# Kernel tuning notes

Hardware: AMD Instinct MI355X
Metric: run time of the kernel (lower is better)

Reference implementation:

```python
import jax, jax.numpy as jnp
import numpy as np

NUM_HEADS = 16

def _rope_tables(T, head_dim):
    # angular_freq: (1/1024)**linspace(0,1,head_dim//4), padded with head_dim//4 zeros
    af = (1.0 / 1024.0) ** jnp.linspace(0.0, 1.0, head_dim // 4, dtype=jnp.float32)
    af = jnp.concatenate([af, jnp.zeros(head_dim // 4, dtype=jnp.float32)])  # [head_dim//2]
    t = jnp.arange(T, dtype=jnp.float32)
    theta = t[:, None] * af[None, :]  # [T, head_dim//2]
    return jnp.cos(theta), jnp.sin(theta)

def _apply_rope(x_bthd, cos, sin):
    # x_bthd: [B,T,H,D]; cos/sin: [T,D//2]
    x1, x2 = jnp.split(x_bthd.astype(jnp.float32), 2, axis=-1)
    c = cos[None, :, None, :]
    s = sin[None, :, None, :]
    y1 = x1 * c + x2 * s
    y2 = -x1 * s + x2 * c
    return jnp.concatenate([y1, y2], axis=-1).astype(x_bthd.dtype)

def setup_inputs() -> dict:
    key = jax.random.key(0)
    k1, k2, k3 = jax.random.split(key, 3)
    B, T, C = 4, 2048, 1024
    std = 0.5 * C ** (-0.5)
    bound = (3.0 ** 0.5) * std
    x = jax.random.normal(k1, (B, T, C), dtype=jnp.float32)
    qkv_w = jax.random.uniform(k2, (3, C, C), dtype=jnp.float32, minval=-bound, maxval=bound)
    c_proj_w = 0.02 * jax.random.normal(k3, (C, C), dtype=jnp.float32)
    c_proj_b = jnp.zeros((C,), dtype=jnp.float32)
    return {"x": x, "qkv_w": qkv_w, "c_proj_w": c_proj_w, "c_proj_b": c_proj_b}

def reference(x, qkv_w, c_proj_w, c_proj_b):
    B, T, C = x.shape
    H = NUM_HEADS
    D = C // H
    # QKV projection: F.linear(x, qkv_w.flatten(end_dim=1)) -> x @ W.T
    qkv = jnp.einsum('btc,nc->btn', x, qkv_w.reshape(3 * C, C))  # [B,T,3C]
    qkv = qkv.reshape(B, T, 3 * H, D)
    q, k, v = jnp.split(qkv, 3, axis=-2)  # each [B,T,H,D]
    cos, sin = _rope_tables(T, D)
    q = _apply_rope(q, cos, sin)
    k = _apply_rope(k, cos, sin)
    # causal SDPA, scale 1/sqrt(D)
    scale = 1.0 / jnp.sqrt(jnp.float32(D))
    scores = jnp.einsum('bqhd,bkhd->bhqk', q, k) * scale  # [B,H,T,T]
    mask = jnp.tril(jnp.ones((T, T), dtype=bool))
    scores = jnp.where(mask[None, None], scores, jnp.finfo(scores.dtype).min)
    attn = jax.nn.softmax(scores, axis=-1)
    y = jnp.einsum('bhqk,bkhd->bqhd', attn, v).reshape(B, T, C)
    return y @ c_proj_w.T + c_proj_b
```

## Files before the change

kernel.cpp:

```cpp
#include <hip/hip_runtime.h>

typedef unsigned short ushort_t;
typedef __bf16 bf16x8 __attribute__((ext_vector_type(8)));
typedef unsigned short ushort8_t __attribute__((ext_vector_type(8)));
typedef unsigned short ushort4_t __attribute__((ext_vector_type(4)));
typedef float floatx4 __attribute__((ext_vector_type(4)));
typedef unsigned int uint4_t __attribute__((ext_vector_type(4)));
typedef unsigned int uint2_t __attribute__((ext_vector_type(2)));

__device__ __forceinline__ ushort_t f2bf(float f) {
    unsigned int u = __float_as_uint(f);
    u += 0x7FFFu + ((u >> 16) & 1u);
    return (ushort_t)(u >> 16);
}
__device__ __forceinline__ float bf2f(ushort_t b) {
    return __uint_as_float(((unsigned int)b) << 16);
}
__device__ __forceinline__ bf16x8 ld_frag(const ushort_t* p) {
    ushort8_t u = *(const ushort8_t*)p;
    return __builtin_bit_cast(bf16x8, u);
}
__device__ __forceinline__ unsigned pack_trunc(float lo, float hi) {
    return __builtin_amdgcn_perm(__float_as_uint(hi), __float_as_uint(lo), 0x07060302u);
}
__device__ __forceinline__ floatx4 mfma16(bf16x8 a, bf16x8 b, floatx4 c) {
    return __builtin_amdgcn_mfma_f32_16x16x32_bf16(a, b, c, 0, 0, 0);
}
__device__ __forceinline__ void async16(const ushort_t* g, ushort_t* l) {
    __builtin_amdgcn_global_load_lds((const __attribute__((address_space(1))) void*)g,
                                     (__attribute__((address_space(3))) void*)l, 16, 0, 0);
}

__global__ __launch_bounds__(256) void cvt_dual(const float* __restrict__ s1,
                                                ushort_t* __restrict__ d1, int n1,
                                                const float* __restrict__ s2,
                                                ushort_t* __restrict__ d2, int n2) {
    int idx = blockIdx.x * 256 + threadIdx.x;
    const float* src;
    ushort_t* dst;
    if (idx < n1) {
        src = s1; dst = d1;
    } else {
        idx -= n1;
        if (idx >= n2) return;
        src = s2; dst = d2;
    }
    const float4* s = (const float4*)src + (size_t)idx * 2;
    float4 a = s[0], b = s[1];
    ushort8_t v;
    v[0] = f2bf(a.x); v[1] = f2bf(a.y); v[2] = f2bf(a.z); v[3] = f2bf(a.w);
    v[4] = f2bf(b.x); v[5] = f2bf(b.y); v[6] = f2bf(b.z); v[7] = f2bf(b.w);
    *(ushort8_t*)(dst + (size_t)idx * 8) = v;
}

template <int MODE>
__global__ __launch_bounds__(256) void gemm_a(const ushort_t* __restrict__ A,
                                              const ushort_t* __restrict__ B,
                                              const float* __restrict__ bias,
                                              void* __restrict__ Cout,
                                              ushort_t* __restrict__ vt,
                                              int M, int N) {
    constexpr int K = 1024;
    __shared__ __attribute__((aligned(16))) ushort_t As[128 * 32];
    __shared__ __attribute__((aligned(16))) ushort_t Bs[128 * 32];
    const int tid = threadIdx.x;
    const int lane = tid & 63, wave = tid >> 6;
    const int quad = lane >> 4, l16 = lane & 15;
    const int wm = wave & 1, wn = wave >> 1;
    const int m0 = blockIdx.y * 128, n0 = blockIdx.x * 128;

    const ushort_t* ga = A + (size_t)(m0 + wave * 32 + (lane >> 2)) * K + (lane & 3) * 8;
    const ushort_t* gb = B + (size_t)(n0 + wave * 32 + (lane >> 2)) * K + (lane & 3) * 8;
    const ushort_t* ga2 = ga + 16 * K;
    const ushort_t* gb2 = gb + 16 * K;
    ushort_t* la = As + wave * 1024;
    ushort_t* lb = Bs + wave * 1024;

    floatx4 acc[4][4] = {};

#pragma unroll
    for (int k0 = 0; k0 < K; k0 += 32) {
        __syncthreads();
        async16(ga + k0, la);
        async16(ga2 + k0, la + 512);
        async16(gb + k0, lb);
        async16(gb2 + k0, lb + 512);
        __syncthreads();

        bf16x8 af[4], bfr[4];
#pragma unroll
        for (int mt = 0; mt < 4; ++mt)
            af[mt] = ld_frag(&As[(wm * 64 + mt * 16 + l16) * 32 + quad * 8]);
#pragma unroll
        for (int nt = 0; nt < 4; ++nt)
            bfr[nt] = ld_frag(&Bs[(wn * 64 + nt * 16 + l16) * 32 + quad * 8]);
#pragma unroll
        for (int mt = 0; mt < 4; ++mt)
#pragma unroll
            for (int nt = 0; nt < 4; ++nt)
                acc[mt][nt] = mfma16(af[mt], bfr[nt], acc[mt][nt]);
    }

    if constexpr (MODE == 2) {
        if (n0 + wn * 64 < 2048) {
            float afreq = exp2f((float)l16 * (-10.0f / 15.0f));
#pragma unroll
            for (int mt = 0; mt < 4; ++mt) {
                int rowb = m0 + wm * 64 + mt * 16 + quad * 4;
#pragma unroll
                for (int r = 0; r < 4; ++r) {
                    int t = (rowb + r) & 2047;
                    float th = (float)t * afreq;
                    float sn, cs;
                    __sincosf(th, &sn, &cs);
                    float q1 = acc[mt][0][r], q2 = acc[mt][2][r];
                    acc[mt][0][r] = q1 * cs + q2 * sn;
                    acc[mt][2][r] = -q1 * sn + q2 * cs;
                }
            }
        }
    }

#pragma unroll
    for (int mt = 0; mt < 4; ++mt) {
        int row = m0 + wm * 64 + mt * 16 + quad * 4;
#pragma unroll
        for (int nt = 0; nt < 4; ++nt) {
            int nglob = n0 + wn * 64 + nt * 16 + l16;
            if constexpr (MODE == 0) {
                float bv = bias ? bias[nglob] : 0.0f;
#pragma unroll
                for (int r = 0; r < 4; ++r)
                    ((float*)Cout)[(size_t)(row + r) * N + nglob] = acc[mt][nt][r] + bv;
            } else {
                if (nglob < 2048) {
#pragma unroll
                    for (int r = 0; r < 4; ++r)
                        ((ushort_t*)Cout)[(size_t)(row + r) * 2048 + nglob] =
                            f2bf(acc[mt][nt][r]);
                } else {
                    int d = nglob & 63, hh = (nglob >> 6) & 15;
                    int bb = row >> 11, t = row & 2047;
                    ushort4_t pk;
                    pk.x = f2bf(acc[mt][nt][0]);
                    pk.y = f2bf(acc[mt][nt][1]);
                    pk.z = f2bf(acc[mt][nt][2]);
                    pk.w = f2bf(acc[mt][nt][3]);
                    *(ushort4_t*)&vt[(((size_t)bb * 16 + hh) * 64 + d) * 2048 + t] = pk;
                }
            }
        }
    }
}

#define ATT_SCALE 0.18033688011112042f

template <bool DIAG>
__device__ __forceinline__ void attn_step(
    const ushort_t* __restrict__ Ks, const ushort_t* __restrict__ Vt,
    ushort_t* __restrict__ Pw, const bf16x8 (&qf)[2][2],
    floatx4 (&o)[2][4], floatx4 (&lac)[2], float (&m_)[2],
    int quad, int l16, int sw8, int mhi, int qrel) {
    ushort8_t ou;
#pragma unroll
    for (int j = 0; j < 8; ++j) ou[j] = 0x3F80;
    const bf16x8 vONE = __builtin_bit_cast(bf16x8, ou);

    floatx4 s[8][2];
    __builtin_amdgcn_s_setprio(1);
#pragma unroll
    for (int mt = 0; mt < 8; ++mt) {
        if (DIAG && mt > mhi) continue;
        const ushort_t* kr = &Ks[(mt * 16 + l16) * 64];
        bf16x8 k0 = ld_frag(kr + ((quad * 8) ^ sw8));
        bf16x8 k1 = ld_frag(kr + ((32 + quad * 8) ^ sw8));
#pragma unroll
        for (int nt = 0; nt < 2; ++nt) {
            floatx4 z = {};
            z = mfma16(k0, qf[nt][0], z);
            s[mt][nt] = mfma16(k1, qf[nt][1], z);
        }
    }
    __builtin_amdgcn_s_setprio(0);

    if (DIAG) {
#pragma unroll
        for (int mt = 0; mt < 8; ++mt) {
            if (mt > mhi) continue;
#pragma unroll
            for (int nt = 0; nt < 2; ++nt)
#pragma unroll
                for (int r = 0; r < 4; ++r)
                    if (mt * 16 + quad * 4 + r > qrel + nt * 16 + l16)
                        s[mt][nt][r] = -3e38f;
        }
    }

    float mx[2];
#pragma unroll
    for (int nt = 0; nt < 2; ++nt) {
        float m0 = -3e38f;
#pragma unroll
        for (int mt = 0; mt < 8; ++mt) {
            if (DIAG && mt > mhi) continue;
            m0 = fmaxf(m0, fmaxf(fmaxf(s[mt][nt][0], s[mt][nt][1]),
                                 fmaxf(s[mt][nt][2], s[mt][nt][3])));
        }
        m0 = fmaxf(m0, __shfl_xor(m0, 16));
        m0 = fmaxf(m0, __shfl_xor(m0, 32));
        mx[nt] = m0;
    }
    bool resc = !__all((mx[0] - m_[0] <= 8.0f) && (mx[1] - m_[1] <= 8.0f));
    if (resc) {
        float alpha_l[2];
#pragma unroll
        for (int nt = 0; nt < 2; ++nt) {
            float mnew = fmaxf(m_[nt], mx[nt]);
            alpha_l[nt] = __builtin_amdgcn_exp2f(m_[nt] - mnew);
            m_[nt] = mnew;
        }
#pragma unroll
        for (int mtq = 0; mtq < 2; ++mtq)
#pragma unroll
            for (int r = 0; r < 4; ++r) {
                float ao = __shfl(alpha_l[mtq], quad * 4 + r);
                lac[mtq][r] *= ao;
#pragma unroll
                for (int ntd = 0; ntd < 4; ++ntd) o[mtq][ntd][r] *= ao;
            }
    }
#pragma unroll
    for (int nt = 0; nt < 2; ++nt)
#pragma unroll
        for (int mt = 0; mt < 8; ++mt) {
            if (DIAG && mt > mhi) continue;
#pragma unroll
            for (int r = 0; r < 4; ++r)
                s[mt][nt][r] = __builtin_amdgcn_exp2f(s[mt][nt][r] - m_[nt]);
        }

#pragma unroll
    for (int half = 0; half < 2; ++half) {
        if (DIAG && 4 * half > mhi) continue;
#pragma unroll
        for (int mt = 4 * half; mt < 4 * half + 4; ++mt) {
            if (DIAG && mt > mhi) continue;
#pragma unroll
            for (int nt = 0; nt < 2; ++nt) {
                uint2_t pk;
                pk.x = pack_trunc(s[mt][nt][0], s[mt][nt][1]);
                pk.y = pack_trunc(s[mt][nt][2], s[mt][nt][3]);
                *(uint2_t*)&Pw[(nt * 16 + l16) * 72 + (mt - 4 * half) * 16 + quad * 4] =
                    pk;
            }
        }

        __builtin_amdgcn_s_setprio(1);
#pragma unroll
        for (int kc2 = 0; kc2 < 2; ++kc2) {
            const int kc = 2 * half + kc2;
            if (DIAG && kc > (mhi >> 1)) continue;
            bf16x8 ap0 = ld_frag(&Pw[l16 * 72 + kc2 * 32 + quad * 8]);
            bf16x8 ap1 = ld_frag(&Pw[(16 + l16) * 72 + kc2 * 32 + quad * 8]);
            lac[0] = mfma16(ap0, vONE, lac[0]);
            lac[1] = mfma16(ap1, vONE, lac[1]);
#pragma unroll
            for (int ntd = 0; ntd < 4; ++ntd) {
                bf16x8 bv = ld_frag(&Vt[(ntd * 16 + l16) * 136 + kc * 32 + quad * 8]);
                o[0][ntd] = mfma16(ap0, bv, o[0][ntd]);
                o[1][ntd] = mfma16(ap1, bv, o[1][ntd]);
            }
        }
        __builtin_amdgcn_s_setprio(0);
    }
}

__global__ __launch_bounds__(256, 2) void attn_kernel(const ushort_t* __restrict__ qk,
                                                      const ushort_t* __restrict__ vt,
                                                      ushort_t* __restrict__ y) {
    __shared__ __attribute__((aligned(16))) ushort_t Ks[128 * 64];
    __shared__ __attribute__((aligned(16))) ushort_t Vt[64 * 136];
    __shared__ __attribute__((aligned(16))) ushort_t Pw_all[4 * 2304];

    const int tid = threadIdx.x, lane = tid & 63, w = tid >> 6;
    const int quad = lane >> 4, l16 = lane & 15;
    const int lrow = lane >> 3, lchunk = lane & 7;
    const int sw8 = 8 * (l16 >> 1);
    ushort_t* Pw = Pw_all + w * 2304;

    const int idx = (int)blockIdx.x;
    const int rank = idx >> 6, bh = idx & 63;
    constexpr int jj_tab[16] = {15, 13, 11, 9, 0, 2, 4, 6, 14, 12, 10, 8, 1, 3, 5, 7};
    const int jj = jj_tab[rank];
    const int b = bh >> 4, h = bh & 15;

    const ushort_t* base_k = qk + (size_t)(b * 2048) * 2048 + 1024 + h * 64;
    const ushort_t* base_v = vt + (size_t)bh * 64 * 2048;
    const int vd = w * 4 + (lane >> 4);
    const int vc8 = lane & 15;

    ushort8_t kreg[4], vreg[4];
    auto load_kv = [&](int kt) {
        const ushort_t* gk = base_k + (size_t)(kt * 128) * 2048 + lchunk * 8;
#pragma unroll
        for (int i = 0; i < 4; ++i)
            kreg[i] = *(const ushort8_t*)(gk + (size_t)(w * 32 + i * 8 + lrow) * 2048);
        const ushort_t* gv = base_v + kt * 128;
#pragma unroll
        for (int i = 0; i < 4; ++i)
            vreg[i] = *(const ushort8_t*)(gv + (size_t)(i * 16 + vd) * 2048 + vc8 * 8);
    };
    auto store_kv = [&]() {
#pragma unroll
        for (int i = 0; i < 4; ++i) {
            int row = w * 32 + i * 8 + lrow;
            *(ushort8_t*)&Ks[row * 64 + 8 * (lchunk ^ ((row >> 1) & 7))] = kreg[i];
        }
#pragma unroll
        for (int i = 0; i < 4; ++i)
            *(ushort8_t*)&Vt[(i * 16 + vd) * 136 + vc8 * 8] = vreg[i];
    };

    const int q0 = jj * 128 + w * 32;

    bf16x8 qf[2][2];
    {
        const ushort_t* qb = qk + (size_t)(b * 2048 + q0) * 2048 + h * 64 + quad * 8;
#pragma unroll
        for (int nt = 0; nt < 2; ++nt)
#pragma unroll
            for (int kd = 0; kd < 2; ++kd) {
                ushort8_t raw =
                    *(const ushort8_t*)(qb + (size_t)(nt * 16 + l16) * 2048 + kd * 32);
                uint4_t dw;
#pragma unroll
                for (int jx = 0; jx < 4; ++jx) {
                    float f0 = bf2f(raw[2 * jx]) * ATT_SCALE;
                    float f1 = bf2f(raw[2 * jx + 1]) * ATT_SCALE;
                    dw[jx] = pack_trunc(f0, f1);
                }
                qf[nt][kd] = __builtin_bit_cast(bf16x8, dw);
            }
    }

    floatx4 o[2][4] = {};
    floatx4 lac[2] = {};
    float m_[2] = {-3e38f, -3e38f};

    load_kv(0);
#pragma unroll 1
    for (int kt = 0; kt <= jj; ++kt) {
        __syncthreads();
        store_kv();
        __syncthreads();
        if (kt < jj) load_kv(kt + 1);

        if (kt < jj)
            attn_step<false>(Ks, Vt, Pw, qf, o, lac, m_, quad, l16, sw8, 7, 0);
        else
            attn_step<true>(Ks, Vt, Pw, qf, o, lac, m_, quad, l16, sw8, 2 * w + 1,
                            w * 32);
    }

    ushort_t* yb = y + (size_t)(b * 2048 + q0) * 1024 + h * 64;
#pragma unroll
    for (int mtq = 0; mtq < 2; ++mtq)
#pragma unroll
        for (int r = 0; r < 4; ++r) {
            float inv = 1.0f / lac[mtq][r];
            int row = mtq * 16 + quad * 4 + r;
#pragma unroll
            for (int ntd = 0; ntd < 4; ++ntd)
                yb[(size_t)row * 1024 + ntd * 16 + l16] = f2bf(o[mtq][ntd][r] * inv);
        }
}

extern "C" void kernel_launch(void* const* d_in, const int* in_sizes, int n_in,
                              void* d_out, int out_size, void* d_ws, size_t ws_size,
                              hipStream_t stream) {
    const float* x = (const float*)d_in[0];
    const float* qkv_w = (const float*)d_in[1];
    const float* c_proj_w = (const float*)d_in[2];
    const float* c_proj_b = (const float*)d_in[3];
    float* out = (float*)d_out;

    const int M = 8192;

    ushort_t* qk = (ushort_t*)d_ws;
    ushort_t* vt = (ushort_t*)((char*)d_ws + (size_t)33554432);
    ushort_t* wpb = vt;
    ushort_t* wb = (ushort_t*)((char*)d_ws + (size_t)50331648);
    ushort_t* y = wb;
    ushort_t* xb = (ushort_t*)d_out;

    cvt_dual<<<dim3(5632), 256, 0, stream>>>(x, xb, M * 1024 / 8,
                                             qkv_w, wb, 3072 * 1024 / 8);

    gemm_a<2><<<dim3(3072 / 128, M / 128), 256, 0, stream>>>(
        xb, wb, nullptr, qk, vt, M, 3072);

    attn_kernel<<<dim3(1024), 256, 0, stream>>>(qk, vt, y);

    cvt_dual<<<dim3(512), 256, 0, stream>>>(c_proj_w, wpb, 1024 * 1024 / 8,
                                            nullptr, nullptr, 0);

    gemm_a<0><<<dim3(1024 / 128, M / 128), 256, 0, stream>>>(
        y, wpb, c_proj_b, out, nullptr, M, 1024);
}
```

Before: 254.5 us.

## Triple-buffer GEMM shared-memory tiles with async prefetch two stages ahead

Replaces the single-buffer load/sync/compute loop in the projection GEMM with a three-stage shared-memory ring. Global-to-LDS async loads run two k-steps ahead, and explicit vmcnt waits plus one barrier per iteration replace the two full syncthreads per step. The goal is to hide global load latency behind MFMA work. It triples LDS usage per block (48KB), which may reduce occupancy, and depends on correct vmcnt accounting for the in-flight async copies.

```diff
diff --git a/kernel.cpp b/kernel.cpp
--- a/kernel.cpp
+++ b/kernel.cpp
@@ -61,8 +61,8 @@
                                               ushort_t* __restrict__ vt,
                                               int M, int N) {
     constexpr int K = 1024;
-    __shared__ __attribute__((aligned(16))) ushort_t As[128 * 32];
-    __shared__ __attribute__((aligned(16))) ushort_t Bs[128 * 32];
+    __shared__ __attribute__((aligned(16))) ushort_t As[3][128 * 32];
+    __shared__ __attribute__((aligned(16))) ushort_t Bs[3][128 * 32];
     const int tid = threadIdx.x;
     const int lane = tid & 63, wave = tid >> 6;
     const int quad = lane >> 4, l16 = lane & 15;
@@ -73,32 +73,53 @@
     const ushort_t* gb = B + (size_t)(n0 + wave * 32 + (lane >> 2)) * K + (lane & 3) * 8;
     const ushort_t* ga2 = ga + 16 * K;
     const ushort_t* gb2 = gb + 16 * K;
-    ushort_t* la = As + wave * 1024;
-    ushort_t* lb = Bs + wave * 1024;
+    const int woff = wave * 1024;
 
     floatx4 acc[4][4] = {};
 
-#pragma unroll
-    for (int k0 = 0; k0 < K; k0 += 32) {
-        __syncthreads();
-        async16(ga + k0, la);
-        async16(ga2 + k0, la + 512);
-        async16(gb + k0, lb);
-        async16(gb2 + k0, lb + 512);
-        __syncthreads();
+    async16(ga, &As[0][woff]);
+    async16(ga2, &As[0][woff] + 512);
+    async16(gb, &Bs[0][woff]);
+    async16(gb2, &Bs[0][woff] + 512);
+    async16(ga + 32, &As[1][woff]);
+    async16(ga2 + 32, &As[1][woff] + 512);
+    async16(gb + 32, &Bs[1][woff]);
+    async16(gb2 + 32, &Bs[1][woff] + 512);
+    asm volatile("s_waitcnt vmcnt(4)" ::: "memory");
+    __builtin_amdgcn_s_barrier();
+
+#pragma unroll
+    for (int t = 0; t < 32; ++t) {
+        const int cb = t % 3;
+        if (t < 30) {
+            const int nb = (t + 2) % 3;
+            const int k1 = (t + 2) * 32;
+            async16(ga + k1, &As[nb][woff]);
+            async16(ga2 + k1, &As[nb][woff] + 512);
+            async16(gb + k1, &Bs[nb][woff]);
+            async16(gb2 + k1, &Bs[nb][woff] + 512);
+        }
 
         bf16x8 af[4], bfr[4];
 #pragma unroll
         for (int mt = 0; mt < 4; ++mt)
-            af[mt] = ld_frag(&As[(wm * 64 + mt * 16 + l16) * 32 + quad * 8]);
+            af[mt] = ld_frag(&As[cb][(wm * 64 + mt * 16 + l16) * 32 + quad * 8]);
 #pragma unroll
         for (int nt = 0; nt < 4; ++nt)
-            bfr[nt] = ld_frag(&Bs[(wn * 64 + nt * 16 + l16) * 32 + quad * 8]);
+            bfr[nt] = ld_frag(&Bs[cb][(wn * 64 + nt * 16 + l16) * 32 + quad * 8]);
 #pragma unroll
         for (int mt = 0; mt < 4; ++mt)
 #pragma unroll
             for (int nt = 0; nt < 4; ++nt)
                 acc[mt][nt] = mfma16(af[mt], bfr[nt], acc[mt][nt]);
+
+        if (t < 31) {
+            if (t < 30)
+                asm volatile("s_waitcnt vmcnt(4)" ::: "memory");
+            else
+                asm volatile("s_waitcnt vmcnt(0)" ::: "memory");
+            __builtin_amdgcn_s_barrier();
+        }
     }
 
     if constexpr (MODE == 2) {
```

Result: slower. 268.8 us (+5.6%).

## Double-buffer GEMM LDS tiles with K=64 stages and XOR swizzle

Applied to the files above, without the earlier changes.

The projection GEMM now uses two LDS buffers and prefetches the next K tile asynchronously while the MFMAs run on the current one. It also doubles the K depth per stage to 64 and XOR-swizzles the LDS columns to avoid bank conflicts, which halves the number of barriers per tile. The cost is four times the LDS (64KB per block), which may reduce occupancy.

```diff
diff --git a/kernel.cpp b/kernel.cpp
--- a/kernel.cpp
+++ b/kernel.cpp
@@ -61,44 +61,64 @@
                                               ushort_t* __restrict__ vt,
                                               int M, int N) {
     constexpr int K = 1024;
-    __shared__ __attribute__((aligned(16))) ushort_t As[128 * 32];
-    __shared__ __attribute__((aligned(16))) ushort_t Bs[128 * 32];
+    __shared__ __attribute__((aligned(16))) ushort_t As[2][128 * 64];
+    __shared__ __attribute__((aligned(16))) ushort_t Bs[2][128 * 64];
     const int tid = threadIdx.x;
     const int lane = tid & 63, wave = tid >> 6;
     const int quad = lane >> 4, l16 = lane & 15;
     const int wm = wave & 1, wn = wave >> 1;
     const int m0 = blockIdx.y * 128, n0 = blockIdx.x * 128;
 
-    const ushort_t* ga = A + (size_t)(m0 + wave * 32 + (lane >> 2)) * K + (lane & 3) * 8;
-    const ushort_t* gb = B + (size_t)(n0 + wave * 32 + (lane >> 2)) * K + (lane & 3) * 8;
-    const ushort_t* ga2 = ga + 16 * K;
-    const ushort_t* gb2 = gb + 16 * K;
-    ushort_t* la = As + wave * 1024;
-    ushort_t* lb = Bs + wave * 1024;
+    const int lr = lane >> 3, lc = lane & 7;
+    const int swc = lc ^ lr;
+    const ushort_t* ga = A + (size_t)(m0 + wave * 32 + lr) * K + swc * 8;
+    const ushort_t* gb = B + (size_t)(n0 + wave * 32 + lr) * K + swc * 8;
+    const int woff = wave * 2048;
 
     floatx4 acc[4][4] = {};
 
-#pragma unroll
-    for (int k0 = 0; k0 < K; k0 += 32) {
-        __syncthreads();
-        async16(ga + k0, la);
-        async16(ga2 + k0, la + 512);
-        async16(gb + k0, lb);
-        async16(gb2 + k0, lb + 512);
-        __syncthreads();
-
-        bf16x8 af[4], bfr[4];
+    const int rsw = (l16 & 7) * 8;
+
+    auto stage = [&](int kt, int buf) {
+#pragma unroll
+        for (int i = 0; i < 4; ++i) {
+            async16(ga + (size_t)kt * 64 + (size_t)i * 8 * K, &As[buf][woff + i * 512]);
+            async16(gb + (size_t)kt * 64 + (size_t)i * 8 * K, &Bs[buf][woff + i * 512]);
+        }
+    };
+
+    stage(0, 0);
+    asm volatile("s_waitcnt vmcnt(0)" ::: "memory");
+    __builtin_amdgcn_s_barrier();
+
+#pragma unroll
+    for (int t = 0; t < 16; ++t) {
+        const int cb = t & 1;
+        if (t < 15) stage(t + 1, cb ^ 1);
+
+        bf16x8 af[4][2], bfr[4][2];
 #pragma unroll
         for (int mt = 0; mt < 4; ++mt)
-            af[mt] = ld_frag(&As[(wm * 64 + mt * 16 + l16) * 32 + quad * 8]);
+#pragma unroll
+            for (int ks = 0; ks < 2; ++ks)
+                af[mt][ks] = ld_frag(
+                    &As[cb][(wm * 64 + mt * 16 + l16) * 64 + ((ks * 32 + quad * 8) ^ rsw)]);
 #pragma unroll
         for (int nt = 0; nt < 4; ++nt)
-            bfr[nt] = ld_frag(&Bs[(wn * 64 + nt * 16 + l16) * 32 + quad * 8]);
+#pragma unroll
+            for (int ks = 0; ks < 2; ++ks)
+                bfr[nt][ks] = ld_frag(
+                    &Bs[cb][(wn * 64 + nt * 16 + l16) * 64 + ((ks * 32 + quad * 8) ^ rsw)]);
 #pragma unroll
         for (int mt = 0; mt < 4; ++mt)
 #pragma unroll
-            for (int nt = 0; nt < 4; ++nt)
-                acc[mt][nt] = mfma16(af[mt], bfr[nt], acc[mt][nt]);
+            for (int nt = 0; nt < 4; ++nt) {
+                acc[mt][nt] = mfma16(af[mt][0], bfr[nt][0], acc[mt][nt]);
+                acc[mt][nt] = mfma16(af[mt][1], bfr[nt][1], acc[mt][nt]);
+            }
+
+        asm volatile("s_waitcnt vmcnt(0)" ::: "memory");
+        __builtin_amdgcn_s_barrier();
     }
 
     if constexpr (MODE == 2) {
```

New measurement: 261.2 us. 2.7% more time.
